# Kernel tuning notes

Measured on AMD Instinct MI355X. Metric: run time of the kernel, lower is better.

Reference implementation:

```python
import jax, jax.numpy as jnp
import numpy as np

B, S, HID = 1, 2048, 4096
N_HEADS, N_KV, HEAD_DIM = 32, 8, 128
N_REP = N_HEADS // N_KV
ROPE_THETA = 10000.0
NEG_INF = -1e9


def setup_inputs() -> dict:
    key = jax.random.key(0)
    ks = jax.random.split(key, 5)
    hidden_states = jax.random.normal(ks[0], (B, S, HID), dtype=jnp.float32)
    Wq = jax.random.normal(ks[1], (HID, N_HEADS * HEAD_DIM), dtype=jnp.float32) * 0.02
    Wk = jax.random.normal(ks[2], (HID, N_KV * HEAD_DIM), dtype=jnp.float32) * 0.02
    Wv = jax.random.normal(ks[3], (HID, N_KV * HEAD_DIM), dtype=jnp.float32) * 0.02
    Wo = jax.random.normal(ks[4], (N_HEADS * HEAD_DIM, HID), dtype=jnp.float32) * 0.02
    # causal additive mask [B, 1, S, S]
    causal = jnp.tril(jnp.ones((S, S), dtype=bool))
    attention_mask = jnp.where(causal, 0.0, NEG_INF).astype(jnp.float32)[None, None]
    position_ids = jnp.broadcast_to(jnp.arange(S, dtype=jnp.int32)[None], (B, S))
    return {
        "hidden_states": hidden_states, "Wq": Wq, "Wk": Wk, "Wv": Wv, "Wo": Wo,
        "attention_mask": attention_mask, "position_ids": position_ids,
    }


def _rotate_half(x):
    half = x.shape[-1] // 2
    return jnp.concatenate([-x[..., half:], x[..., :half]], axis=-1)


def _rope_tables(position_ids):
    # inv_freq: [head_dim/2]
    inv_freq = 1.0 / (ROPE_THETA ** (jnp.arange(0, HEAD_DIM, 2, dtype=jnp.float32) / HEAD_DIM))
    # freqs: [B, S, head_dim/2]
    freqs = position_ids.astype(jnp.float32)[..., None] * inv_freq
    emb = jnp.concatenate([freqs, freqs], axis=-1)  # [B, S, head_dim]
    # [B, 1, S, head_dim] to broadcast over heads
    return jnp.cos(emb)[:, None], jnp.sin(emb)[:, None]


def reference(hidden_states, Wq, Wk, Wv, Wo, attention_mask, position_ids):
    b, s, _ = hidden_states.shape
    # projections -> [B, H, S, D]
    q = (hidden_states @ Wq).reshape(b, s, N_HEADS, HEAD_DIM).transpose(0, 2, 1, 3)
    k = (hidden_states @ Wk).reshape(b, s, N_KV, HEAD_DIM).transpose(0, 2, 1, 3)
    v = (hidden_states @ Wv).reshape(b, s, N_KV, HEAD_DIM).transpose(0, 2, 1, 3)
    cos, sin = _rope_tables(position_ids)
    q = q * cos + _rotate_half(q) * sin
    k = k * cos + _rotate_half(k) * sin
    # GQA repeat_kv (repeat_interleave over head dim)
    k = jnp.repeat(k, N_REP, axis=1)
    v = jnp.repeat(v, N_REP, axis=1)
    scores = jnp.einsum("bhqd,bhkd->bhqk", q, k) / jnp.sqrt(jnp.float32(HEAD_DIM))
    scores = scores + attention_mask
    probs = jax.nn.softmax(scores.astype(jnp.float32), axis=-1).astype(q.dtype)
    attn = jnp.einsum("bhqk,bhkd->bhqd", probs, v)
    attn = attn.transpose(0, 2, 1, 3).reshape(b, s, N_HEADS * HEAD_DIM)
    return attn @ Wo
```

## Files before the change

kernel.cpp:

```cpp
#include <hip/hip_runtime.h>
#include <hip/hip_bf16.h>

#define S_LEN 2048
#define HIDDEN 4096
#define NH 32
#define NKV 8
#define HD 128
#define NQKV 6144

typedef __bf16 bf16_t;
typedef __bf16 bf16x8 __attribute__((ext_vector_type(8)));
typedef __bf16 bf16x4 __attribute__((ext_vector_type(4)));
typedef float f32x4 __attribute__((ext_vector_type(4)));

typedef __attribute__((address_space(1))) void gvoid;
typedef __attribute__((address_space(3))) void lvoid;

__device__ __forceinline__ void gload_lds16(const void* g, void* l) {
    __builtin_amdgcn_global_load_lds((gvoid*)g, (lvoid*)l, 16, 0, 0);
}

__device__ __forceinline__ float fast_exp2(float x) {
    return __builtin_amdgcn_exp2f(x);
}

__device__ __forceinline__ unsigned int pack2_bf16(float lo, float hi) {
    bf16_t l = (bf16_t)lo, h = (bf16_t)hi;
    unsigned short lu, hu;
    __builtin_memcpy(&lu, &l, 2);
    __builtin_memcpy(&hu, &h, 2);
    return ((unsigned int)hu << 16) | (unsigned int)lu;
}

__global__ void cast_bf16_kernel(const float* __restrict__ in, bf16_t* __restrict__ out, int n4) {
    int stride = gridDim.x * blockDim.x;
    for (int idx = blockIdx.x * blockDim.x + threadIdx.x; idx < n4; idx += stride) {
        float4 v = ((const float4*)in)[idx];
        bf16x4 o;
        o.x = (bf16_t)v.x; o.y = (bf16_t)v.y; o.z = (bf16_t)v.z; o.w = (bf16_t)v.w;
        ((bf16x4*)out)[idx] = o;
    }
}

__global__ __launch_bounds__(256) void transpose_cast_kernel(const float* __restrict__ in,
                                                             bf16_t* __restrict__ out,
                                                             int ldin, int ldout) {
    __shared__ unsigned int t2[64][34];
    const int c0 = blockIdx.x * 64, r0 = blockIdx.y * 64;
    const int t = threadIdx.x;
    const int tx4 = t & 15, tp = t >> 4;
#pragma unroll
    for (int i = 0; i < 2; ++i) {
        int rp = tp + i * 16;
        const float* p0 = &in[(size_t)(r0 + 2 * rp) * ldin + c0 + tx4 * 4];
        float4 a = *(const float4*)p0;
        float4 b = *(const float4*)(p0 + ldin);
        t2[tx4 * 4 + 0][rp] = pack2_bf16(a.x, b.x);
        t2[tx4 * 4 + 1][rp] = pack2_bf16(a.y, b.y);
        t2[tx4 * 4 + 2][rp] = pack2_bf16(a.z, b.z);
        t2[tx4 * 4 + 3][rp] = pack2_bf16(a.w, b.w);
    }
    __syncthreads();
    const int q = t & 3, cc = t >> 2;
    uint2 v0 = *(const uint2*)&t2[cc][q * 8 + 0];
    uint2 v1 = *(const uint2*)&t2[cc][q * 8 + 2];
    uint2 v2 = *(const uint2*)&t2[cc][q * 8 + 4];
    uint2 v3 = *(const uint2*)&t2[cc][q * 8 + 6];
    bf16_t* o = &out[(size_t)(c0 + cc) * ldout + r0 + q * 16];
    *(uint4*)o = make_uint4(v0.x, v0.y, v1.x, v1.y);
    *(uint4*)(o + 8) = make_uint4(v2.x, v2.y, v3.x, v3.y);
}

__global__ __launch_bounds__(256) void transpose_bf16_kernel(const bf16_t* __restrict__ in,
                                                             bf16_t* __restrict__ out,
                                                             int ldin, int ldout) {
    __shared__ unsigned int t2[64][34];
    const int c0 = blockIdx.x * 64, r0 = blockIdx.y * 64;
    const int t = threadIdx.x;
    const int tx4 = t & 15, tp = t >> 4;
#pragma unroll
    for (int i = 0; i < 2; ++i) {
        int rp = tp + i * 16;
        const bf16_t* p0 = &in[(size_t)(r0 + 2 * rp) * ldin + c0 + tx4 * 4];
        bf16x4 a = *(const bf16x4*)p0;
        bf16x4 b = *(const bf16x4*)(p0 + ldin);
#pragma unroll
        for (int k2 = 0; k2 < 4; ++k2) {
            unsigned short lu, hu;
            bf16_t la = a[k2], hb = b[k2];
            __builtin_memcpy(&lu, &la, 2);
            __builtin_memcpy(&hu, &hb, 2);
            t2[tx4 * 4 + k2][rp] = ((unsigned int)hu << 16) | (unsigned int)lu;
        }
    }
    __syncthreads();
    const int q = t & 3, cc = t >> 2;
    uint2 v0 = *(const uint2*)&t2[cc][q * 8 + 0];
    uint2 v1 = *(const uint2*)&t2[cc][q * 8 + 2];
    uint2 v2 = *(const uint2*)&t2[cc][q * 8 + 4];
    uint2 v3 = *(const uint2*)&t2[cc][q * 8 + 6];
    bf16_t* o = &out[(size_t)(c0 + cc) * ldout + r0 + q * 16];
    *(uint4*)o = make_uint4(v0.x, v0.y, v1.x, v1.y);
    *(uint4*)(o + 8) = make_uint4(v2.x, v2.y, v3.x, v3.y);
}

template<int BN, typename OutT>
__global__ __launch_bounds__(512, 2) void gemm_ring_kernel(const bf16_t* __restrict__ A,
                                                           const bf16_t* __restrict__ Bt,
                                                           OutT* __restrict__ C,
                                                           int M, int N, int K) {
    constexpr int NF = BN / 64;
    constexpr int VMN = (BN == 256) ? 3 : 2;
    __shared__ bf16_t As[3][128 * 32];
    __shared__ bf16_t Bs[3][BN * 32];
    const int tid = threadIdx.x;
    const int lane = tid & 63, w = tid >> 6;
    const int wm = w >> 2, wn = w & 3;
    const int g = lane >> 4, c16 = lane & 15;
    const int srow = lane >> 2;
    const int scg = ((lane & 3) ^ ((lane >> 3) & 3)) * 8;
    const int rdc = (g ^ ((c16 >> 1) & 3)) * 8;

    const int nbm = M / 128;
    const int cpx = gridDim.x >> 3;
    const int bid = blockIdx.x;
    const int swz = (bid & 7) * cpx + (bid >> 3);
    const int bm = swz % nbm, bn = swz / nbm;

    const bf16_t* Ab = A + (size_t)(bm * 128) * K;
    const bf16_t* Bb = Bt + (size_t)bn * BN * K;

    auto stage = [&](int slot, int kt) {
        const bf16_t* Ak = Ab + (size_t)kt * 32;
        const bf16_t* Bk = Bb + (size_t)kt * 32;
        if constexpr (BN == 256) {
            int rb = 16 * w;
            gload_lds16(Ak + (size_t)(rb + srow) * K + scg, &As[slot][rb * 32]);
#pragma unroll
            for (int j = 0; j < 2; ++j) {
                int rb2 = 32 * w + 16 * j;
                gload_lds16(Bk + (size_t)(rb2 + srow) * K + scg, &Bs[slot][rb2 * 32]);
            }
        } else if constexpr (BN == 192) {
            if (w < 4) {
#pragma unroll
                for (int j = 0; j < 3; ++j) {
                    int rb = 48 * w + 16 * j;
                    gload_lds16(Bk + (size_t)(rb + srow) * K + scg, &Bs[slot][rb * 32]);
                }
            } else {
#pragma unroll
                for (int j = 0; j < 2; ++j) {
                    int rb = 32 * (w - 4) + 16 * j;
                    gload_lds16(Ak + (size_t)(rb + srow) * K + scg, &As[slot][rb * 32]);
                }
            }
        } else {
            int rb = 16 * w;
            gload_lds16(Ak + (size_t)(rb + srow) * K + scg, &As[slot][rb * 32]);
            gload_lds16(Bk + (size_t)(rb + srow) * K + scg, &Bs[slot][rb * 32]);
        }
    };

    f32x4 acc[4][NF];
#pragma unroll
    for (int i = 0; i < 4; ++i)
#pragma unroll
        for (int j = 0; j < NF; ++j)
            acc[i][j] = (f32x4){0.f, 0.f, 0.f, 0.f};

    const int NT = K / 32;
    stage(0, 0);
    stage(1, 1);

    int slot = 0, slot2 = 2;
    for (int t = 0; t < NT; ++t) {
        asm volatile("s_waitcnt vmcnt(%0)" :: "n"(VMN) : "memory");
        __builtin_amdgcn_s_barrier();
        __builtin_amdgcn_sched_barrier(0);
        __builtin_amdgcn_s_setprio(1);

        bf16x8 af[4], bf[NF];
#pragma unroll
        for (int i = 0; i < 4; ++i) {
            int arow = wm * 64 + i * 16 + c16;
            af[i] = *(const bf16x8*)&As[slot][arow * 32 + rdc];
        }
#pragma unroll
        for (int j = 0; j < NF; ++j) {
            int brow = wn * (BN / 4) + j * 16 + c16;
            bf[j] = *(const bf16x8*)&Bs[slot][brow * 32 + rdc];
        }
        int nk = t + 2;
        if (nk >= NT) nk -= NT;
        stage(slot2, nk);

#pragma unroll
        for (int i = 0; i < 4; ++i)
#pragma unroll
            for (int j = 0; j < NF; ++j)
                acc[i][j] = __builtin_amdgcn_mfma_f32_16x16x32_bf16(af[i], bf[j], acc[i][j], 0, 0, 0);
        __builtin_amdgcn_s_setprio(0);

        slot = (slot + 1) % 3;
        slot2 = (slot2 + 1) % 3;
    }

#pragma unroll
    for (int mi = 0; mi < 4; ++mi)
#pragma unroll
        for (int ni = 0; ni < NF; ++ni) {
            int col = bn * BN + wn * (BN / 4) + ni * 16 + c16;
#pragma unroll
            for (int r = 0; r < 4; ++r) {
                int row = bm * 128 + wm * 64 + mi * 16 + g * 4 + r;
                C[(size_t)row * N + col] = (OutT)acc[mi][ni][r];
            }
        }
}

__global__ void rope_kernel(const bf16_t* __restrict__ in, bf16_t* __restrict__ out,
                            const int* __restrict__ pos, int H, int ld, float scale) {
    int idx = blockIdx.x * blockDim.x + threadIdx.x;
    int total = S_LEN * H * 64;
    if (idx >= total) return;
    int d = idx & 63;
    int h = (idx >> 6) % H;
    int s = idx / (64 * H);
    const bf16_t* base = in + (size_t)s * ld + h * HD;
    float x0 = (float)base[d], x1 = (float)base[d + 64];
    float p = (float)pos[s];
    float invf = fast_exp2(-0.20762050593046935f * (float)d);
    float f = p * invf;
    float sn, cs;
    __sincosf(f, &sn, &cs);
    float o0 = (x0 * cs - x1 * sn) * scale;
    float o1 = (x1 * cs + x0 * sn) * scale;
    bf16_t* ob = out + ((size_t)h * S_LEN + s) * HD;
    ob[d] = (bf16_t)o0;
    ob[d + 64] = (bf16_t)o1;
}

#define PLD 68
__global__ __launch_bounds__(512) void attn_kernel(const bf16_t* __restrict__ Q,
                                                   const bf16_t* __restrict__ K,
                                                   const bf16_t* __restrict__ Vt,
                                                   bf16_t* __restrict__ O) {
    __shared__ bf16_t Ks[2][64 * 128];
    __shared__ bf16_t Vs[2][128 * 64];
    __shared__ bf16_t Pl[8][16 * PLD];
    const int tid = threadIdx.x;
    const int lane = tid & 63, w = tid >> 6;
    const int bid = blockIdx.x;
    const int h = bid & 31;
    const int x = bid >> 5;
    const int wg = w >> 2, wi = w & 3;
    const int qtile = wg == 0 ? x : 15 - x;
    const int qb = qtile * 128 + wi * 32;
    const int kv = h >> 2;
    const int g = lane >> 4, c16 = lane & 15;
    const int c7 = c16 & 7;
    const bf16_t* Qh = Q + (size_t)h * S_LEN * HD;
    const bf16_t* Kh = K + (size_t)kv * S_LEN * HD;
    const bf16_t* Vh = Vt + (size_t)kv * HD * S_LEN;
    bf16_t* P = Pl[w];

    auto stage = [&](int buf, int kb) {
        bf16_t* Kd = Ks[buf];
        bf16_t* Vd = Vs[buf];
#pragma unroll
        for (int j = 0; j < 2; ++j) {
            int i = w * 2 + j;
            {
                int row = 4 * i + (lane >> 4);
                int sc = (lane & 15) ^ (row & 7);
                gload_lds16(Kh + (size_t)(kb + row) * HD + sc * 8, Kd + i * 512);
            }
            {
                int row = 8 * i + (lane >> 3);
                int sc = (lane & 7) ^ ((lane >> 3) & 7);
                gload_lds16(Vh + (size_t)row * S_LEN + kb + sc * 8, Vd + i * 512);
            }
        }
    };

    bf16x8 qf[2][4];
#pragma unroll
    for (int rg = 0; rg < 2; ++rg)
#pragma unroll
        for (int c = 0; c < 4; ++c)
            qf[rg][c] = *(const bf16x8*)(Qh + (size_t)(qb + rg * 16 + c16) * HD + c * 32 + g * 8);

    bf16x8 ones;
#pragma unroll
    for (int j = 0; j < 8; ++j) ones[j] = (bf16_t)1.0f;

    f32x4 acc_o[2][8];
#pragma unroll
    for (int rg = 0; rg < 2; ++rg)
#pragma unroll
        for (int dt = 0; dt < 8; ++dt) acc_o[rg][dt] = (f32x4){0.f, 0.f, 0.f, 0.f};
    f32x4 acc_l[2] = {(f32x4){0.f, 0.f, 0.f, 0.f}, (f32x4){0.f, 0.f, 0.f, 0.f}};
    float m[2][4];
#pragma unroll
    for (int rg = 0; rg < 2; ++rg)
#pragma unroll
        for (int r = 0; r < 4; ++r) m[rg][r] = -1e30f;

    const int nkt = 32 - 2 * x;
    stage(0, 0);
    __syncthreads();
    int cur = 0;

    bf16x8 pf[2][2];
    for (int kt = 0; kt < nkt; ++kt) {
        if (kt + 1 < nkt) stage(cur ^ 1, (kt + 1) * 64);
        const int kb = kt * 64;
        const bf16_t* Kb = Ks[cur];
        const bf16_t* Vb = Vs[cur];

        if (kb <= qb + 31) {
            const bool diag = (kb + 63 > qb);

            f32x4 sacc[2][4];
#pragma unroll
            for (int rg = 0; rg < 2; ++rg)
#pragma unroll
                for (int t = 0; t < 4; ++t) sacc[rg][t] = (f32x4){0.f, 0.f, 0.f, 0.f};
#pragma unroll
            for (int t = 0; t < 4; ++t) {
                const bf16_t* krow = Kb + (t * 16 + c16) * 128;
#pragma unroll
                for (int cc = 0; cc < 4; ++cc) {
                    bf16x8 kf = *(const bf16x8*)(krow + (((cc * 4 + g) ^ c7) * 8));
                    sacc[0][t] = __builtin_amdgcn_mfma_f32_16x16x32_bf16(qf[0][cc], kf, sacc[0][t], 0, 0, 0);
                    sacc[1][t] = __builtin_amdgcn_mfma_f32_16x16x32_bf16(qf[1][cc], kf, sacc[1][t], 0, 0, 0);
                }
            }
#pragma unroll
            for (int rg = 0; rg < 2; ++rg) {
                float p[4][4], mxr[4];
#pragma unroll
                for (int r = 0; r < 4; ++r) {
                    int qq = qb + rg * 16 + g * 4 + r;
#pragma unroll
                    for (int t = 0; t < 4; ++t) {
                        float sv = sacc[rg][t][r];
                        if (diag && (kb + t * 16 + c16 > qq)) sv = -1e30f;
                        p[t][r] = sv;
                    }
                    float mx = fmaxf(fmaxf(p[0][r], p[1][r]), fmaxf(p[2][r], p[3][r]));
                    mx = fmaxf(mx, __shfl_xor(mx, 1));
                    mx = fmaxf(mx, __shfl_xor(mx, 2));
                    mx = fmaxf(mx, __shfl_xor(mx, 4));
                    mx = fmaxf(mx, __shfl_xor(mx, 8));
                    mxr[r] = mx;
                }
                bool resc = false;
#pragma unroll
                for (int r = 0; r < 4; ++r) resc = resc || (mxr[r] > m[rg][r] + 8.f);
                if (__any(resc)) {
#pragma unroll
                    for (int r = 0; r < 4; ++r) {
                        float mn = fmaxf(m[rg][r], mxr[r]);
                        float al = fast_exp2(m[rg][r] - mn);
                        m[rg][r] = mn;
                        acc_l[rg][r] *= al;
#pragma unroll
                        for (int dt = 0; dt < 8; ++dt) acc_o[rg][dt][r] *= al;
                    }
                }
#pragma unroll
                for (int r = 0; r < 4; ++r)
#pragma unroll
                    for (int t = 0; t < 4; ++t)
                        p[t][r] = fast_exp2(p[t][r] - m[rg][r]);
#pragma unroll
                for (int t = 0; t < 4; ++t)
#pragma unroll
                    for (int r = 0; r < 4; ++r)
                        P[(g * 4 + r) * PLD + t * 16 + c16] = (bf16_t)p[t][r];
                pf[rg][0] = *(const bf16x8*)(P + c16 * PLD + g * 8);
                pf[rg][1] = *(const bf16x8*)(P + c16 * PLD + 32 + g * 8);
            }
            acc_l[0] = __builtin_amdgcn_mfma_f32_16x16x32_bf16(pf[0][0], ones, acc_l[0], 0, 0, 0);
            acc_l[0] = __builtin_amdgcn_mfma_f32_16x16x32_bf16(pf[0][1], ones, acc_l[0], 0, 0, 0);
            acc_l[1] = __builtin_amdgcn_mfma_f32_16x16x32_bf16(pf[1][0], ones, acc_l[1], 0, 0, 0);
            acc_l[1] = __builtin_amdgcn_mfma_f32_16x16x32_bf16(pf[1][1], ones, acc_l[1], 0, 0, 0);
#pragma unroll
            for (int dt = 0; dt < 8; ++dt) {
                const bf16_t* vrow = Vb + (dt * 16 + c16) * 64;
                bf16x8 vf0 = *(const bf16x8*)(vrow + ((g ^ c7) * 8));
                bf16x8 vf1 = *(const bf16x8*)(vrow + (((4 + g) ^ c7) * 8));
                acc_o[0][dt] = __builtin_amdgcn_mfma_f32_16x16x32_bf16(pf[0][0], vf0, acc_o[0][dt], 0, 0, 0);
                acc_o[0][dt] = __builtin_amdgcn_mfma_f32_16x16x32_bf16(pf[0][1], vf1, acc_o[0][dt], 0, 0, 0);
                acc_o[1][dt] = __builtin_amdgcn_mfma_f32_16x16x32_bf16(pf[1][0], vf0, acc_o[1][dt], 0, 0, 0);
                acc_o[1][dt] = __builtin_amdgcn_mfma_f32_16x16x32_bf16(pf[1][1], vf1, acc_o[1][dt], 0, 0, 0);
            }
        }
        __syncthreads();
        cur ^= 1;
    }
#pragma unroll
    for (int rg = 0; rg < 2; ++rg) {
        float inv_l[4];
#pragma unroll
        for (int r = 0; r < 4; ++r) inv_l[r] = 1.f / acc_l[rg][r];
#pragma unroll
        for (int dt = 0; dt < 8; ++dt)
#pragma unroll
            for (int r = 0; r < 4; ++r)
                O[(size_t)(qb + rg * 16 + g * 4 + r) * HIDDEN + h * HD + dt * 16 + c16] =
                    (bf16_t)(acc_o[rg][dt][r] * inv_l[r]);
    }
}

extern "C" void kernel_launch(void* const* d_in, const int* in_sizes, int n_in,
                              void* d_out, int out_size, void* d_ws, size_t ws_size,
                              hipStream_t stream) {
    const float* hs = (const float*)d_in[0];
    const float* Wq = (const float*)d_in[1];
    const float* Wk = (const float*)d_in[2];
    const float* Wv = (const float*)d_in[3];
    const float* Wo = (const float*)d_in[4];
    const int* pos = (const int*)d_in[6];
    float* out = (float*)d_out;

    char* ws = (char*)d_ws;
    size_t off = 0;
    auto alloc = [&](size_t bytes) -> void* {
        void* p = ws + off;
        off += (bytes + 255) & ~(size_t)255;
        return p;
    };
    bf16_t* hB    = (bf16_t*)alloc((size_t)S_LEN * HIDDEN * 2);
    bf16_t* WqkvT = (bf16_t*)alloc((size_t)NQKV * HIDDEN * 2);
    bf16_t* WoT   = (bf16_t*)alloc((size_t)HIDDEN * HIDDEN * 2);
    bf16_t* QKV   = (bf16_t*)alloc((size_t)S_LEN * NQKV * 2);
    bf16_t* Qr    = (bf16_t*)alloc((size_t)NH * S_LEN * HD * 2);
    bf16_t* Kr    = (bf16_t*)alloc((size_t)NKV * S_LEN * HD * 2);
    bf16_t* Vt    = (bf16_t*)alloc((size_t)NKV * HD * S_LEN * 2);
    bf16_t* Oat   = (bf16_t*)alloc((size_t)S_LEN * HIDDEN * 2);

    cast_bf16_kernel<<<2048, 256, 0, stream>>>(hs, hB, S_LEN * HIDDEN / 4);
    transpose_cast_kernel<<<dim3(HIDDEN / 64, HIDDEN / 64), 256, 0, stream>>>(Wq, WqkvT, HIDDEN, HIDDEN);
    transpose_cast_kernel<<<dim3(1024 / 64, HIDDEN / 64), 256, 0, stream>>>(Wk, WqkvT + (size_t)4096 * HIDDEN, 1024, HIDDEN);
    transpose_cast_kernel<<<dim3(1024 / 64, HIDDEN / 64), 256, 0, stream>>>(Wv, WqkvT + (size_t)5120 * HIDDEN, 1024, HIDDEN);
    transpose_cast_kernel<<<dim3(HIDDEN / 64, HIDDEN / 64), 256, 0, stream>>>(Wo, WoT, HIDDEN, HIDDEN);
    gemm_ring_kernel<192, bf16_t><<<(S_LEN / 128) * (NQKV / 192), 512, 0, stream>>>(hB, WqkvT, QKV, S_LEN, NQKV, HIDDEN);
    rope_kernel<<<(S_LEN * NH * 64 + 255) / 256, 256, 0, stream>>>(QKV, Qr, pos, NH, NQKV, 0.1275174310f);
    rope_kernel<<<(S_LEN * NKV * 64 + 255) / 256, 256, 0, stream>>>(QKV + 4096, Kr, pos, NKV, NQKV, 1.0f);
    transpose_bf16_kernel<<<dim3(1024 / 64, S_LEN / 64), 256, 0, stream>>>(QKV + 5120, Vt, NQKV, S_LEN);
    attn_kernel<<<256, 512, 0, stream>>>(Qr, Kr, Vt, Oat);
    gemm_ring_kernel<128, float><<<(S_LEN / 128) * (HIDDEN / 128), 512, 0, stream>>>(Oat, WoT, out, S_LEN, HIDDEN, HIDDEN);
}
```

Baseline: 365.8 us.

## Split KV tiles across warp groups per query tile and merge partial softmax

The attention kernel used to give its two warp groups different query tiles (x and 15-x), so the group with the shorter causal range sat idle for much of the shared KV loop. Now both groups work on the same query tile in two sequential phases. Each group takes alternating 64-key tiles from a 4-slot shared-memory ring, and at the end the two partial (m, l, O) states are merged through shared memory. This is meant to balance work across waves and cut idle wavefronts. In exchange it adds an extra barrier, an LDS merge step per phase and a larger LDS footprint of roughly 145KB.

Result: faster. 347.1 us (-5.1%).

```diff
diff --git a/kernel.cpp b/kernel.cpp
--- a/kernel.cpp
+++ b/kernel.cpp
@@ -246,28 +246,26 @@
                                                    const bf16_t* __restrict__ K,
                                                    const bf16_t* __restrict__ Vt,
                                                    bf16_t* __restrict__ O) {
-    __shared__ bf16_t Ks[2][64 * 128];
-    __shared__ bf16_t Vs[2][128 * 64];
+    __shared__ bf16_t Ks[4][64 * 128];
+    __shared__ bf16_t Vs[4][128 * 64];
     __shared__ bf16_t Pl[8][16 * PLD];
     const int tid = threadIdx.x;
     const int lane = tid & 63, w = tid >> 6;
     const int bid = blockIdx.x;
     const int h = bid & 31;
     const int x = bid >> 5;
-    const int wg = w >> 2, wi = w & 3;
-    const int qtile = wg == 0 ? x : 15 - x;
-    const int qb = qtile * 128 + wi * 32;
+    const int grp = w >> 2, wi = w & 3;
     const int kv = h >> 2;
-    const int g = lane >> 4, c16 = lane & 15;
+    const int quad = lane >> 4, c16 = lane & 15;
     const int c7 = c16 & 7;
     const bf16_t* Qh = Q + (size_t)h * S_LEN * HD;
     const bf16_t* Kh = K + (size_t)kv * S_LEN * HD;
     const bf16_t* Vh = Vt + (size_t)kv * HD * S_LEN;
     bf16_t* P = Pl[w];
 
-    auto stage = [&](int buf, int kb) {
-        bf16_t* Kd = Ks[buf];
-        bf16_t* Vd = Vs[buf];
+    auto stage = [&](int slot, int kb) {
+        bf16_t* Kd = Ks[slot];
+        bf16_t* Vd = Vs[slot];
 #pragma unroll
         for (int j = 0; j < 2; ++j) {
             int i = w * 2 + j;
@@ -284,134 +282,174 @@
         }
     };
 
-    bf16x8 qf[2][4];
-#pragma unroll
-    for (int rg = 0; rg < 2; ++rg)
-#pragma unroll
-        for (int c = 0; c < 4; ++c)
-            qf[rg][c] = *(const bf16x8*)(Qh + (size_t)(qb + rg * 16 + c16) * HD + c * 32 + g * 8);
-
     bf16x8 ones;
 #pragma unroll
     for (int j = 0; j < 8; ++j) ones[j] = (bf16_t)1.0f;
 
-    f32x4 acc_o[2][8];
-#pragma unroll
-    for (int rg = 0; rg < 2; ++rg)
-#pragma unroll
-        for (int dt = 0; dt < 8; ++dt) acc_o[rg][dt] = (f32x4){0.f, 0.f, 0.f, 0.f};
-    f32x4 acc_l[2] = {(f32x4){0.f, 0.f, 0.f, 0.f}, (f32x4){0.f, 0.f, 0.f, 0.f}};
-    float m[2][4];
-#pragma unroll
-    for (int rg = 0; rg < 2; ++rg)
-#pragma unroll
-        for (int r = 0; r < 4; ++r) m[rg][r] = -1e30f;
-
-    const int nkt = 32 - 2 * x;
-    stage(0, 0);
-    __syncthreads();
-    int cur = 0;
-
-    bf16x8 pf[2][2];
-    for (int kt = 0; kt < nkt; ++kt) {
-        if (kt + 1 < nkt) stage(cur ^ 1, (kt + 1) * 64);
-        const int kb = kt * 64;
-        const bf16_t* Kb = Ks[cur];
-        const bf16_t* Vb = Vs[cur];
-
-        if (kb <= qb + 31) {
-            const bool diag = (kb + 63 > qb);
-
-            f32x4 sacc[2][4];
+    for (int ph = 0; ph < 2; ++ph) {
+        const int qt = (ph == 0) ? x : 15 - x;
+        const int R = qt + 1;
+        const int qb = qt * 128 + wi * 32;
+
+        bf16x8 qf[2][4];
+#pragma unroll
+        for (int rg = 0; rg < 2; ++rg)
+#pragma unroll
+            for (int c = 0; c < 4; ++c)
+                qf[rg][c] = *(const bf16x8*)(Qh + (size_t)(qb + rg * 16 + c16) * HD + c * 32 + quad * 8);
+
+        f32x4 acc_o[2][8];
+#pragma unroll
+        for (int rg = 0; rg < 2; ++rg)
+#pragma unroll
+            for (int dt = 0; dt < 8; ++dt) acc_o[rg][dt] = (f32x4){0.f, 0.f, 0.f, 0.f};
+        f32x4 acc_l[2] = {(f32x4){0.f, 0.f, 0.f, 0.f}, (f32x4){0.f, 0.f, 0.f, 0.f}};
+        float m[2][4];
+#pragma unroll
+        for (int rg = 0; rg < 2; ++rg)
+#pragma unroll
+            for (int r = 0; r < 4; ++r) m[rg][r] = -1e30f;
+
+        stage(0, 0);
+        stage(1, 64);
+        __syncthreads();
+
+        for (int r = 0; r < R; ++r) {
+            int jn0 = 2 * r + 2, jn1 = 2 * r + 3;
+            if (jn0 < 2 * R) stage(jn0 & 3, jn0 * 64);
+            if (jn1 < 2 * R) stage(jn1 & 3, jn1 * 64);
+
+            const int j = 2 * r + grp;
+            const int kb = j * 64;
+            const bf16_t* Kb = Ks[j & 3];
+            const bf16_t* Vb = Vs[j & 3];
+
+            if (kb <= qb + 31) {
+                const bool diag = (kb + 63 > qb);
+
+                f32x4 sacc[2][4];
+#pragma unroll
+                for (int rg = 0; rg < 2; ++rg)
+#pragma unroll
+                    for (int t = 0; t < 4; ++t) sacc[rg][t] = (f32x4){0.f, 0.f, 0.f, 0.f};
+#pragma unroll
+                for (int t = 0; t < 4; ++t) {
+                    const bf16_t* krow = Kb + (t * 16 + c16) * 128;
+#pragma unroll
+                    for (int cc = 0; cc < 4; ++cc) {
+                        bf16x8 kf = *(const bf16x8*)(krow + (((cc * 4 + quad) ^ c7) * 8));
+                        sacc[0][t] = __builtin_amdgcn_mfma_f32_16x16x32_bf16(qf[0][cc], kf, sacc[0][t], 0, 0, 0);
+                        sacc[1][t] = __builtin_amdgcn_mfma_f32_16x16x32_bf16(qf[1][cc], kf, sacc[1][t], 0, 0, 0);
+                    }
+                }
+                bf16x8 pf[2][2];
+#pragma unroll
+                for (int rg = 0; rg < 2; ++rg) {
+                    float p[4][4], mxr[4];
+#pragma unroll
+                    for (int r4 = 0; r4 < 4; ++r4) {
+                        int qq = qb + rg * 16 + quad * 4 + r4;
+#pragma unroll
+                        for (int t = 0; t < 4; ++t) {
+                            float sv = sacc[rg][t][r4];
+                            if (diag && (kb + t * 16 + c16 > qq)) sv = -1e30f;
+                            p[t][r4] = sv;
+                        }
+                        float mx = fmaxf(fmaxf(p[0][r4], p[1][r4]), fmaxf(p[2][r4], p[3][r4]));
+                        mx = fmaxf(mx, __shfl_xor(mx, 1));
+                        mx = fmaxf(mx, __shfl_xor(mx, 2));
+                        mx = fmaxf(mx, __shfl_xor(mx, 4));
+                        mx = fmaxf(mx, __shfl_xor(mx, 8));
+                        mxr[r4] = mx;
+                    }
+                    bool resc = false;
+#pragma unroll
+                    for (int r4 = 0; r4 < 4; ++r4) resc = resc || (mxr[r4] > m[rg][r4] + 8.f);
+                    if (__any(resc)) {
+#pragma unroll
+                        for (int r4 = 0; r4 < 4; ++r4) {
+                            float mn = fmaxf(m[rg][r4], mxr[r4]);
+                            float al = fast_exp2(m[rg][r4] - mn);
+                            m[rg][r4] = mn;
+                            acc_l[rg][r4] *= al;
+#pragma unroll
+                            for (int dt = 0; dt < 8; ++dt) acc_o[rg][dt][r4] *= al;
+                        }
+                    }
+#pragma unroll
+                    for (int r4 = 0; r4 < 4; ++r4)
+#pragma unroll
+                        for (int t = 0; t < 4; ++t)
+                            p[t][r4] = fast_exp2(p[t][r4] - m[rg][r4]);
+#pragma unroll
+                    for (int t = 0; t < 4; ++t)
+#pragma unroll
+                        for (int r4 = 0; r4 < 4; ++r4)
+                            P[(quad * 4 + r4) * PLD + t * 16 + c16] = (bf16_t)p[t][r4];
+                    pf[rg][0] = *(const bf16x8*)(P + c16 * PLD + quad * 8);
+                    pf[rg][1] = *(const bf16x8*)(P + c16 * PLD + 32 + quad * 8);
+                }
+                acc_l[0] = __builtin_amdgcn_mfma_f32_16x16x32_bf16(pf[0][0], ones, acc_l[0], 0, 0, 0);
+                acc_l[0] = __builtin_amdgcn_mfma_f32_16x16x32_bf16(pf[0][1], ones, acc_l[0], 0, 0, 0);
+                acc_l[1] = __builtin_amdgcn_mfma_f32_16x16x32_bf16(pf[1][0], ones, acc_l[1], 0, 0, 0);
+                acc_l[1] = __builtin_amdgcn_mfma_f32_16x16x32_bf16(pf[1][1], ones, acc_l[1], 0, 0, 0);
+#pragma unroll
+                for (int dt = 0; dt < 8; ++dt) {
+                    const bf16_t* vrow = Vb + (dt * 16 + c16) * 64;
+                    bf16x8 vf0 = *(const bf16x8*)(vrow + ((quad ^ c7) * 8));
+                    bf16x8 vf1 = *(const bf16x8*)(vrow + (((4 + quad) ^ c7) * 8));
+                    acc_o[0][dt] = __builtin_amdgcn_mfma_f32_16x16x32_bf16(pf[0][0], vf0, acc_o[0][dt], 0, 0, 0);
+                    acc_o[0][dt] = __builtin_amdgcn_mfma_f32_16x16x32_bf16(pf[0][1], vf1, acc_o[0][dt], 0, 0, 0);
+                    acc_o[1][dt] = __builtin_amdgcn_mfma_f32_16x16x32_bf16(pf[1][0], vf0, acc_o[1][dt], 0, 0, 0);
+                    acc_o[1][dt] = __builtin_amdgcn_mfma_f32_16x16x32_bf16(pf[1][1], vf1, acc_o[1][dt], 0, 0, 0);
+                }
+            }
+            __syncthreads();
+        }
+
+        float* s0 = (float*)&Ks[0][0];
+        float* s1 = (float*)&Vs[0][0];
+        const int sl = wi * 64 + lane;
+        if (grp == 1) {
 #pragma unroll
             for (int rg = 0; rg < 2; ++rg)
 #pragma unroll
-                for (int t = 0; t < 4; ++t) sacc[rg][t] = (f32x4){0.f, 0.f, 0.f, 0.f};
-#pragma unroll
-            for (int t = 0; t < 4; ++t) {
-                const bf16_t* krow = Kb + (t * 16 + c16) * 128;
-#pragma unroll
-                for (int cc = 0; cc < 4; ++cc) {
-                    bf16x8 kf = *(const bf16x8*)(krow + (((cc * 4 + g) ^ c7) * 8));
-                    sacc[0][t] = __builtin_amdgcn_mfma_f32_16x16x32_bf16(qf[0][cc], kf, sacc[0][t], 0, 0, 0);
-                    sacc[1][t] = __builtin_amdgcn_mfma_f32_16x16x32_bf16(qf[1][cc], kf, sacc[1][t], 0, 0, 0);
-                }
-            }
-#pragma unroll
-            for (int rg = 0; rg < 2; ++rg) {
-                float p[4][4], mxr[4];
-#pragma unroll
-                for (int r = 0; r < 4; ++r) {
-                    int qq = qb + rg * 16 + g * 4 + r;
-#pragma unroll
-                    for (int t = 0; t < 4; ++t) {
-                        float sv = sacc[rg][t][r];
-                        if (diag && (kb + t * 16 + c16 > qq)) sv = -1e30f;
-                        p[t][r] = sv;
+                for (int r4 = 0; r4 < 4; ++r4) {
+                    s0[(rg * 4 + r4) * 256 + sl] = m[rg][r4];
+                    s0[(8 + rg * 4 + r4) * 256 + sl] = acc_l[rg][r4];
+                }
+#pragma unroll
+            for (int dt = 0; dt < 8; ++dt)
+#pragma unroll
+                for (int r4 = 0; r4 < 4; ++r4) {
+                    s0[(16 + dt * 4 + r4) * 256 + sl] = acc_o[0][dt][r4];
+                    s1[(dt * 4 + r4) * 256 + sl] = acc_o[1][dt][r4];
+                }
+        }
+        __syncthreads();
+        if (grp == 0) {
+#pragma unroll
+            for (int rg = 0; rg < 2; ++rg)
+#pragma unroll
+                for (int r4 = 0; r4 < 4; ++r4) {
+                    float m1 = s0[(rg * 4 + r4) * 256 + sl];
+                    float l1 = s0[(8 + rg * 4 + r4) * 256 + sl];
+                    float mm = fmaxf(m[rg][r4], m1);
+                    float a0 = fast_exp2(m[rg][r4] - mm);
+                    float a1 = fast_exp2(m1 - mm);
+                    float ll = acc_l[rg][r4] * a0 + l1 * a1;
+                    float inv = 1.f / ll;
+                    bf16_t* orow = &O[(size_t)(qb + rg * 16 + quad * 4 + r4) * HIDDEN + h * HD];
+#pragma unroll
+                    for (int dt = 0; dt < 8; ++dt) {
+                        float o1 = (rg == 0) ? s0[(16 + dt * 4 + r4) * 256 + sl]
+                                             : s1[(dt * 4 + r4) * 256 + sl];
+                        float val = (acc_o[rg][dt][r4] * a0 + o1 * a1) * inv;
+                        orow[dt * 16 + c16] = (bf16_t)val;
                     }
-                    float mx = fmaxf(fmaxf(p[0][r], p[1][r]), fmaxf(p[2][r], p[3][r]));
-                    mx = fmaxf(mx, __shfl_xor(mx, 1));
-                    mx = fmaxf(mx, __shfl_xor(mx, 2));
-                    mx = fmaxf(mx, __shfl_xor(mx, 4));
-                    mx = fmaxf(mx, __shfl_xor(mx, 8));
-                    mxr[r] = mx;
-                }
-                bool resc = false;
-#pragma unroll
-                for (int r = 0; r < 4; ++r) resc = resc || (mxr[r] > m[rg][r] + 8.f);
-                if (__any(resc)) {
-#pragma unroll
-                    for (int r = 0; r < 4; ++r) {
-                        float mn = fmaxf(m[rg][r], mxr[r]);
-                        float al = fast_exp2(m[rg][r] - mn);
-                        m[rg][r] = mn;
-                        acc_l[rg][r] *= al;
-#pragma unroll
-                        for (int dt = 0; dt < 8; ++dt) acc_o[rg][dt][r] *= al;
-                    }
-                }
-#pragma unroll
-                for (int r = 0; r < 4; ++r)
-#pragma unroll
-                    for (int t = 0; t < 4; ++t)
-                        p[t][r] = fast_exp2(p[t][r] - m[rg][r]);
-#pragma unroll
-                for (int t = 0; t < 4; ++t)
-#pragma unroll
-                    for (int r = 0; r < 4; ++r)
-                        P[(g * 4 + r) * PLD + t * 16 + c16] = (bf16_t)p[t][r];
-                pf[rg][0] = *(const bf16x8*)(P + c16 * PLD + g * 8);
-                pf[rg][1] = *(const bf16x8*)(P + c16 * PLD + 32 + g * 8);
-            }
-            acc_l[0] = __builtin_amdgcn_mfma_f32_16x16x32_bf16(pf[0][0], ones, acc_l[0], 0, 0, 0);
-            acc_l[0] = __builtin_amdgcn_mfma_f32_16x16x32_bf16(pf[0][1], ones, acc_l[0], 0, 0, 0);
-            acc_l[1] = __builtin_amdgcn_mfma_f32_16x16x32_bf16(pf[1][0], ones, acc_l[1], 0, 0, 0);
-            acc_l[1] = __builtin_amdgcn_mfma_f32_16x16x32_bf16(pf[1][1], ones, acc_l[1], 0, 0, 0);
-#pragma unroll
-            for (int dt = 0; dt < 8; ++dt) {
-                const bf16_t* vrow = Vb + (dt * 16 + c16) * 64;
-                bf16x8 vf0 = *(const bf16x8*)(vrow + ((g ^ c7) * 8));
-                bf16x8 vf1 = *(const bf16x8*)(vrow + (((4 + g) ^ c7) * 8));
-                acc_o[0][dt] = __builtin_amdgcn_mfma_f32_16x16x32_bf16(pf[0][0], vf0, acc_o[0][dt], 0, 0, 0);
-                acc_o[0][dt] = __builtin_amdgcn_mfma_f32_16x16x32_bf16(pf[0][1], vf1, acc_o[0][dt], 0, 0, 0);
-                acc_o[1][dt] = __builtin_amdgcn_mfma_f32_16x16x32_bf16(pf[1][0], vf0, acc_o[1][dt], 0, 0, 0);
-                acc_o[1][dt] = __builtin_amdgcn_mfma_f32_16x16x32_bf16(pf[1][1], vf1, acc_o[1][dt], 0, 0, 0);
-            }
+                }
         }
         __syncthreads();
-        cur ^= 1;
-    }
-#pragma unroll
-    for (int rg = 0; rg < 2; ++rg) {
-        float inv_l[4];
-#pragma unroll
-        for (int r = 0; r < 4; ++r) inv_l[r] = 1.f / acc_l[rg][r];
-#pragma unroll
-        for (int dt = 0; dt < 8; ++dt)
-#pragma unroll
-            for (int r = 0; r < 4; ++r)
-                O[(size_t)(qb + rg * 16 + g * 4 + r) * HIDDEN + h * HD + dt * 16 + c16] =
-                    (bf16_t)(acc_o[rg][dt][r] * inv_l[r]);
     }
 }
 
```
